# Kernel optimization log

Measured on AMD Instinct MI355X. Metric: run time of the kernel, lower is better.

## Reference

```python
import jax, jax.numpy as jnp
import numpy as np

B, C, H, W = 1, 448, 64, 64
K, M, PAD, STRIDE = 7, 7, 3, 1
CG = C // K          # key/query channels (KeyQueryMap divides by k) = 64
GP_HID = int(0.5 * CG)  # geometry prior hidden channels = 32
K2 = K * K
CENTER = K2 // 2


def conv1x1(x, w, b):
    # x: (B, Cin, H, W), w: (Cout, Cin), b: (Cout,)
    return jnp.einsum('bchw,oc->bohw', x, w) + b[None, :, None, None]


def unfold(x):
    # torch.nn.Unfold(K, dilation=1, padding=PAD, stride=STRIDE)
    # output layout: (B, Cin*K2, L) with dim1 index = c*K2 + (di*K + dj)
    Bc, Cc, Hc, Wc = x.shape
    xp = jnp.pad(x, ((0, 0), (0, 0), (PAD, PAD), (PAD, PAD)))
    Ho = (Hc + 2 * PAD - K) // STRIDE + 1
    Wo = (Wc + 2 * PAD - K) // STRIDE + 1
    patches = [xp[:, :, di:di + Ho * STRIDE:STRIDE, dj:dj + Wo * STRIDE:STRIDE]
               for di in range(K) for dj in range(K)]
    u = jnp.stack(patches, axis=2)  # (B, Cc, K2, Ho, Wo)
    return u.reshape(Bc, Cc * K2, Ho * Wo), Ho, Wo


def geometry_prior(gp_w1, gp_b1, gp_w2, gp_b2):
    ar = jnp.arange(-(K // 2), K // 2 + 1, dtype=jnp.float32)   # -3..3
    x_pos = jnp.broadcast_to(ar[None, :], (K, K))
    y_pos = jnp.broadcast_to(ar[::-1][:, None], (K, K))          # 3..-3 down rows
    pos = jnp.stack([x_pos, y_pos], axis=0)[None]                # (1, 2, K, K)
    h = jax.nn.relu(conv1x1(pos, gp_w1, gp_b1))
    out = conv1x1(h, gp_w2, gp_b2)                               # (1, CG, K, K)
    return out.reshape(1, CG, 1, K2)


def setup_inputs() -> dict:
    key = jax.random.key(0)
    ks = jax.random.split(key, 12)
    def lin(k, cout, cin):
        return jax.random.normal(k, (cout, cin), jnp.float32) / np.sqrt(cin)
    inp = {
        'x': jax.random.normal(ks[0], (B, C, H, W), jnp.float32),
        'Wk': lin(ks[1], CG, C), 'bk': jnp.zeros((CG,), jnp.float32),
        'Wq': lin(ks[2], CG, C), 'bq': jnp.zeros((CG,), jnp.float32),
        'gp_w1': lin(ks[3], GP_HID, 2), 'gp_b1': jax.random.normal(ks[4], (GP_HID,), jnp.float32) * 0.01,
        'gp_w2': lin(ks[5], CG, GP_HID), 'gp_b2': jax.random.normal(ks[6], (CG,), jnp.float32) * 0.01,
        'Wf': lin(ks[7], C, C), 'bf': jnp.zeros((C,), jnp.float32),
    }
    return inp


def reference(x, Wk, bk, Wq, bq, gp_w1, gp_b1, gp_w2, gp_b2, Wf, bf):
    gpk = geometry_prior(gp_w1, gp_b1, gp_w2, gp_b2)        # (1, CG, 1, K2)
    km = conv1x1(x, Wk, bk)                                  # (B, CG, H, W)
    qm = conv1x1(x, Wq, bq)
    ku, Ho, Wo = unfold(km)
    L = Ho * Wo
    ku = ku.reshape(B, CG, L, K2)   # same row-major semantics as torch .view
    qu, _, _ = unfold(qm)
    qu = qu.reshape(B, CG, L, K2)
    ak = ku * qu[:, :, :, CENTER:CENTER + 1]                 # (B, CG, L, K2)
    ck = jax.nn.softmax(ak + gpk, axis=-1)                   # (B, CG, L, K2)
    xu, _, _ = unfold(x)
    xu = xu.reshape(B, M, C // M, L, K2)                     # (B, M, CG, L, K2)
    # ck broadcasts over the M axis (valid since B == 1); sum over window dim
    pre = jnp.einsum('bglp,bmglp->bmgl', ck, xu).reshape(B, C, Ho, Wo)
    return conv1x1(pre, Wf, bf)
```

## Files before the change

### kernel.cpp

```cpp
#include <hip/hip_runtime.h>
#include <hip/hip_bf16.h>

#define CC   448
#define CGC  64
#define MMM  7
#define HWSZ 4096
#define KK2  49
#define GPH  32

typedef __attribute__((ext_vector_type(8))) short   short8;
typedef __attribute__((ext_vector_type(4))) float   f32x4;
typedef __attribute__((ext_vector_type(4))) unsigned short us4;

__device__ __forceinline__ unsigned short f2b(float f) {
    union { __hip_bfloat16 h; unsigned short u; } cv;
    cv.h = __float2bfloat16(f);
    return cv.u;
}

__global__ __launch_bounds__(256) void kq_mfma(
    const float* __restrict__ x,
    const float* __restrict__ Wk, const float* __restrict__ bk,
    const float* __restrict__ Wq, const float* __restrict__ bq,
    float* __restrict__ km, float* __restrict__ qm)
{
    __shared__ unsigned short As[4096];
    __shared__ unsigned short Bs[512];

    const int tid  = threadIdx.x;
    const int nT   = blockIdx.x * 16;
    const int lane = tid & 63;
    const int wid  = tid >> 6;
    const int wm   = wid * 32;
    const int l15  = lane & 15;
    const int l4   = lane >> 4;

    const int ar  = tid >> 3;
    const int ak  = tid & 7;
    const int bkr = tid >> 3;
    const int bn2 = tid & 7;

    f32x4 acc[2];
    acc[0] = (f32x4){0.f, 0.f, 0.f, 0.f};
    acc[1] = (f32x4){0.f, 0.f, 0.f, 0.f};

    float4 a0 = *(const float4*)(Wk + (size_t)ar * CC + ak * 4);
    float4 a1 = *(const float4*)(Wk + (size_t)(ar + 32) * CC + ak * 4);
    float4 a2 = *(const float4*)(Wq + (size_t)ar * CC + ak * 4);
    float4 a3 = *(const float4*)(Wq + (size_t)(ar + 32) * CC + ak * 4);
    float2 b0 = *(const float2*)(x + (size_t)bkr * HWSZ + nT + bn2 * 2);

    for (int kt = 0; kt < 14; ++kt) {
        {
            int kg = ak >> 1, jo = (ak & 1) * 4;
            us4 w;
            w = (us4){ f2b(a0.x), f2b(a0.y), f2b(a0.z), f2b(a0.w) };
            *(us4*)&As[kg * 1024 + (ar +  0) * 8 + jo] = w;
            w = (us4){ f2b(a1.x), f2b(a1.y), f2b(a1.z), f2b(a1.w) };
            *(us4*)&As[kg * 1024 + (ar + 32) * 8 + jo] = w;
            w = (us4){ f2b(a2.x), f2b(a2.y), f2b(a2.z), f2b(a2.w) };
            *(us4*)&As[kg * 1024 + (ar + 64) * 8 + jo] = w;
            w = (us4){ f2b(a3.x), f2b(a3.y), f2b(a3.z), f2b(a3.w) };
            *(us4*)&As[kg * 1024 + (ar + 96) * 8 + jo] = w;
            int base = (bkr >> 3) * 128 + bn2 * 16 + (bkr & 7);
            Bs[base]     = f2b(b0.x);
            Bs[base + 8] = f2b(b0.y);
        }
        __syncthreads();
        if (kt < 13) {
            int ko = (kt + 1) * 32;
            a0 = *(const float4*)(Wk + (size_t)ar * CC + ko + ak * 4);
            a1 = *(const float4*)(Wk + (size_t)(ar + 32) * CC + ko + ak * 4);
            a2 = *(const float4*)(Wq + (size_t)ar * CC + ko + ak * 4);
            a3 = *(const float4*)(Wq + (size_t)(ar + 32) * CC + ko + ak * 4);
            b0 = *(const float2*)(x + (size_t)(ko + bkr) * HWSZ + nT + bn2 * 2);
        }
        short8 fa0 = *(short8*)&As[l4 * 1024 + (wm + l15) * 8];
        short8 fa1 = *(short8*)&As[l4 * 1024 + (wm + 16 + l15) * 8];
        short8 fb0 = *(short8*)&Bs[l4 * 128 + l15 * 8];
        acc[0] = __builtin_amdgcn_mfma_f32_16x16x32_bf16(fa0, fb0, acc[0], 0, 0, 0);
        acc[1] = __builtin_amdgcn_mfma_f32_16x16x32_bf16(fa1, fb0, acc[1], 0, 0, 0);
        __syncthreads();
    }
    const bool isK = (wid < 2);
    float*       Cd   = isK ? km : qm;
    const float* bias = isK ? bk : bq;
    const int rbase = wm & 63;
    #pragma unroll
    for (int wm2 = 0; wm2 < 2; ++wm2)
        #pragma unroll
        for (int r = 0; r < 4; ++r) {
            int row = rbase + wm2 * 16 + l4 * 4 + r;
            int col = nT + l15;
            Cd[(size_t)row * HWSZ + col] = acc[wm2][r] + bias[row];
        }
}

__global__ __launch_bounds__(256) void fconv_mfma(
    const float* __restrict__ pre,
    const float* __restrict__ Wf, const float* __restrict__ bfv,
    float* __restrict__ out)
{
    __shared__ unsigned short As[2048];
    __shared__ unsigned short Bs[1024];

    const int tid  = threadIdx.x;
    const int nT   = blockIdx.x * 32;
    const int oT   = blockIdx.y * 64;
    const int lane = tid & 63;
    const int wid  = tid >> 6;
    const int l15  = lane & 15;
    const int l4   = lane >> 4;

    const int ar  = tid >> 3;
    const int ak  = tid & 7;
    const int bkr = tid >> 3;
    const int bn4 = tid & 7;

    const float* __restrict__ A = Wf + (size_t)oT * CC;

    f32x4 acc[2];
    acc[0] = (f32x4){0.f, 0.f, 0.f, 0.f};
    acc[1] = (f32x4){0.f, 0.f, 0.f, 0.f};

    float4 a0 = *(const float4*)(A + (size_t)ar * CC + ak * 4);
    float4 a1 = *(const float4*)(A + (size_t)(ar + 32) * CC + ak * 4);
    float4 b0 = *(const float4*)(pre + (size_t)bkr * HWSZ + nT + bn4 * 4);

    for (int kt = 0; kt < 14; ++kt) {
        {
            int kg = ak >> 1, jo = (ak & 1) * 4;
            us4 w;
            w = (us4){ f2b(a0.x), f2b(a0.y), f2b(a0.z), f2b(a0.w) };
            *(us4*)&As[kg * 512 + (ar +  0) * 8 + jo] = w;
            w = (us4){ f2b(a1.x), f2b(a1.y), f2b(a1.z), f2b(a1.w) };
            *(us4*)&As[kg * 512 + (ar + 32) * 8 + jo] = w;
            int base = (bkr >> 3) * 256 + bn4 * 32 + (bkr & 7);
            Bs[base]      = f2b(b0.x);
            Bs[base + 8]  = f2b(b0.y);
            Bs[base + 16] = f2b(b0.z);
            Bs[base + 24] = f2b(b0.w);
        }
        __syncthreads();
        if (kt < 13) {
            int ko = (kt + 1) * 32;
            a0 = *(const float4*)(A + (size_t)ar * CC + ko + ak * 4);
            a1 = *(const float4*)(A + (size_t)(ar + 32) * CC + ko + ak * 4);
            b0 = *(const float4*)(pre + (size_t)(ko + bkr) * HWSZ + nT + bn4 * 4);
        }
        short8 fa  = *(short8*)&As[l4 * 512 + (wid * 16 + l15) * 8];
        short8 fb0 = *(short8*)&Bs[l4 * 256 + l15 * 8];
        short8 fb1 = *(short8*)&Bs[l4 * 256 + (16 + l15) * 8];
        acc[0] = __builtin_amdgcn_mfma_f32_16x16x32_bf16(fa, fb0, acc[0], 0, 0, 0);
        acc[1] = __builtin_amdgcn_mfma_f32_16x16x32_bf16(fa, fb1, acc[1], 0, 0, 0);
        __syncthreads();
    }
    #pragma unroll
    for (int wn2 = 0; wn2 < 2; ++wn2)
        #pragma unroll
        for (int r = 0; r < 4; ++r) {
            int row = oT + wid * 16 + l4 * 4 + r;
            int col = nT + wn2 * 16 + l15;
            out[(size_t)row * HWSZ + col] = acc[wn2][r] + bfv[row];
        }
}

#define GLO 196
#define GHI 260
#define XWORDS (GLO + HWSZ + GHI)

__device__ __forceinline__ int win_off_global(int n, bool& ok) {
    int p  = n >> 12;
    int l  = n & 4095;
    int di = (p * 37) >> 8;
    int dj = p - di * 7;
    int i  = (l >> 6) + di - 3;
    int j  = (l & 63) + dj - 3;
    ok = ((unsigned)i < 64u) && ((unsigned)j < 64u);
    return i * 64 + j;
}

__global__ __launch_bounds__(512, 4) void attn_kernel(
    const float* __restrict__ km, const float* __restrict__ qm,
    const float* __restrict__ x,
    const float* __restrict__ gw1, const float* __restrict__ gb1,
    const float* __restrict__ gw2, const float* __restrict__ gb2,
    float* __restrict__ pre)
{
    __shared__ float klin[XWORDS];
    __shared__ float xlin[XWORDS];
    __shared__ float gpk_s[KK2];
    const int tid = threadIdx.x;
    const int g   = blockIdx.y;
    const int lp  = blockIdx.x * 512 + tid;

    if (tid < 114) {
        float4 z = {0.f, 0.f, 0.f, 0.f};
        int w = (tid < 49) ? tid * 4 : (GLO + HWSZ + (tid - 49) * 4);
        *(float4*)&klin[w] = z;
        *(float4*)&xlin[w] = z;
    }
    {
        const float4* km4 = (const float4*)(km + (size_t)g * HWSZ);
        *(float4*)&klin[GLO + tid * 4]         = km4[tid];
        *(float4*)&klin[GLO + (tid + 512) * 4] = km4[tid + 512];
    }
    if (tid < KK2) {
        int di = tid / 7, dj = tid - di * 7;
        float xp = (float)(dj - 3);
        float yp = (float)(3 - di);
        float acc = gb2[g];
        #pragma unroll
        for (int j = 0; j < GPH; ++j) {
            float h = gw1[j * 2 + 0] * xp + gw1[j * 2 + 1] * yp + gb1[j];
            h = fmaxf(h, 0.f);
            acc = fmaf(gw2[g * GPH + j], h, acc);
        }
        gpk_s[tid] = acc;
    }

    float qc;
    { bool ok; int o = win_off_global(lp * KK2 + 24, ok); qc = ok ? qm[(size_t)g * HWSZ + o] : 0.f; }

    const int n0 = lp * KK2;
    const int p0 = n0 >> 12;
    const int l0 = n0 & 4095;
    const int ts = ((p0 + 1) << 12) - n0;
    const int di0 = (p0 * 37) >> 8, dj0 = p0 - di0 * 7;
    const int p1  = p0 + 1;
    const int di1 = (p1 * 37) >> 8, dj1 = p1 - di1 * 7;
    const int djm3_0 = dj0 - 3, djm3_1 = dj1 - 3;
    const int B0 = GLO + l0 + (di0 - 3) * 64 + djm3_0;
    const int B1 = GLO + l0 - 4096 + (di1 - 3) * 64 + djm3_1;

    float4 xr0, xr1;
    {
        const float4* xg4 = (const float4*)(x + (size_t)g * HWSZ);
        xr0 = xg4[tid]; xr1 = xg4[tid + 512];
    }
    __syncthreads();

    float a[KK2];
    float mx = -1e30f;
    #pragma unroll
    for (int t = 0; t < KK2; ++t) {
        bool s1 = (t >= ts);
        int base = s1 ? B1 : B0;
        float kv = klin[base + t];
        int jj = ((l0 + t) & 63) + (s1 ? djm3_1 : djm3_0);
        kv = ((unsigned)jj < 64u) ? kv : 0.f;
        float av = fmaf(kv, qc, gpk_s[t]);
        a[t] = av;
        mx = fmaxf(mx, av);
    }
    float d = 0.f;
    #pragma unroll
    for (int t = 0; t < KK2; ++t) {
        float e = __expf(a[t] - mx);
        d += e;
        bool s1 = (t >= ts);
        int jj = ((l0 + t) & 63) + (s1 ? djm3_1 : djm3_0);
        a[t] = ((unsigned)jj < 64u) ? e : 0.f;
    }
    const float inv = 1.f / d;

    #pragma unroll 1
    for (int m = 0; m < MMM; ++m) {
        __syncthreads();
        *(float4*)&xlin[GLO + tid * 4]         = xr0;
        *(float4*)&xlin[GLO + (tid + 512) * 4] = xr1;
        __syncthreads();
        if (m < MMM - 1) {
            const float4* xg4 = (const float4*)(x + (size_t)((m + 1) * CGC + g) * HWSZ);
            xr0 = xg4[tid]; xr1 = xg4[tid + 512];
        }
        float acc = 0.f;
        #pragma unroll
        for (int t = 0; t < KK2; ++t) {
            int base = (t >= ts) ? B1 : B0;
            acc = fmaf(a[t], xlin[base + t], acc);
        }
        pre[(size_t)(m * CGC + g) * HWSZ + lp] = acc * inv;
    }
}

extern "C" void kernel_launch(void* const* d_in, const int* in_sizes, int n_in,
                              void* d_out, int out_size, void* d_ws, size_t ws_size,
                              hipStream_t stream) {
    const float* x   = (const float*)d_in[0];
    const float* Wk  = (const float*)d_in[1];
    const float* bk  = (const float*)d_in[2];
    const float* Wq  = (const float*)d_in[3];
    const float* bq  = (const float*)d_in[4];
    const float* gw1 = (const float*)d_in[5];
    const float* gb1 = (const float*)d_in[6];
    const float* gw2 = (const float*)d_in[7];
    const float* gb2 = (const float*)d_in[8];
    const float* Wf  = (const float*)d_in[9];
    const float* bfv = (const float*)d_in[10];
    float* out = (float*)d_out;

    float* km  = (float*)d_ws;
    float* qm  = km + CGC * HWSZ;
    float* pre = qm + CGC * HWSZ;

    kq_mfma    <<<dim3(256),    256, 0, stream>>>(x, Wk, bk, Wq, bq, km, qm);
    attn_kernel<<<dim3(8, CGC), 512, 0, stream>>>(km, qm, x, gw1, gb1, gw2, gb2, pre);
    fconv_mfma <<<dim3(128, 7), 256, 0, stream>>>(pre, Wf, bfv, out);
}
```

Baseline: 115.7 us.

## Stage all x channel pages in LDS and fuse softmax with weighted sum

Result: no change. 114.1 us (-1.5%).

```diff
diff --git a/kernel.cpp b/kernel.cpp
--- a/kernel.cpp
+++ b/kernel.cpp
@@ -167,60 +167,60 @@
 
 #define GLO 196
 #define GHI 260
-#define XWORDS (GLO + HWSZ + GHI)
-
-__device__ __forceinline__ int win_off_global(int n, bool& ok) {
-    int p  = n >> 12;
-    int l  = n & 4095;
-    int di = (p * 37) >> 8;
-    int dj = p - di * 7;
-    int i  = (l >> 6) + di - 3;
-    int j  = (l & 63) + dj - 3;
-    ok = ((unsigned)i < 64u) && ((unsigned)j < 64u);
-    return i * 64 + j;
-}
-
-__global__ __launch_bounds__(512, 4) void attn_kernel(
+#define PGW (GLO + HWSZ + GHI)
+#define NPG 8
+
+__global__ __launch_bounds__(1024, 4) void attn_kernel(
     const float* __restrict__ km, const float* __restrict__ qm,
     const float* __restrict__ x,
     const float* __restrict__ gw1, const float* __restrict__ gb1,
     const float* __restrict__ gw2, const float* __restrict__ gb2,
     float* __restrict__ pre)
 {
-    __shared__ float klin[XWORDS];
-    __shared__ float xlin[XWORDS];
+    __shared__ __align__(16) float sm[NPG * PGW];
     __shared__ float gpk_s[KK2];
+
     const int tid = threadIdx.x;
     const int g   = blockIdx.y;
-    const int lp  = blockIdx.x * 512 + tid;
-
-    if (tid < 114) {
-        float4 z = {0.f, 0.f, 0.f, 0.f};
-        int w = (tid < 49) ? tid * 4 : (GLO + HWSZ + (tid - 49) * 4);
-        *(float4*)&klin[w] = z;
-        *(float4*)&xlin[w] = z;
+    const int lp  = blockIdx.x * 1024 + tid;
+
+    if (tid < NPG * 114) {
+        int page = tid / 114;
+        int r    = tid - page * 114;
+        int w    = (r < 49) ? r * 4 : (GLO + HWSZ + (r - 49) * 4);
+        *(float4*)&sm[page * PGW + w] = (float4){0.f, 0.f, 0.f, 0.f};
     }
     {
-        const float4* km4 = (const float4*)(km + (size_t)g * HWSZ);
-        *(float4*)&klin[GLO + tid * 4]         = km4[tid];
-        *(float4*)&klin[GLO + (tid + 512) * 4] = km4[tid + 512];
+        const float4* s0 = (const float4*)(km + (size_t)g * HWSZ);
+        *(float4*)&sm[GLO + tid * 4] = s0[tid];
+        #pragma unroll
+        for (int m = 0; m < MMM; ++m) {
+            const float4* sx = (const float4*)(x + (size_t)(m * CGC + g) * HWSZ);
+            *(float4*)&sm[(m + 1) * PGW + GLO + tid * 4] = sx[tid];
+        }
     }
     if (tid < KK2) {
         int di = tid / 7, dj = tid - di * 7;
         float xp = (float)(dj - 3);
         float yp = (float)(3 - di);
-        float acc = gb2[g];
+        float a2 = gb2[g];
         #pragma unroll
         for (int j = 0; j < GPH; ++j) {
-            float h = gw1[j * 2 + 0] * xp + gw1[j * 2 + 1] * yp + gb1[j];
-            h = fmaxf(h, 0.f);
-            acc = fmaf(gw2[g * GPH + j], h, acc);
-        }
-        gpk_s[tid] = acc;
+            float h = fmaxf(gw1[j * 2 + 0] * xp + gw1[j * 2 + 1] * yp + gb1[j], 0.f);
+            a2 = fmaf(gw2[g * GPH + j], h, a2);
+        }
+        gpk_s[tid] = a2;
     }
 
     float qc;
-    { bool ok; int o = win_off_global(lp * KK2 + 24, ok); qc = ok ? qm[(size_t)g * HWSZ + o] : 0.f; }
+    {
+        int nc = lp * KK2 + 24;
+        int pc = nc >> 12, lc = nc & 4095;
+        int dic = (pc * 37) >> 8, djc = pc - dic * 7;
+        int i = (lc >> 6) + dic - 3, j = (lc & 63) + djc - 3;
+        bool ok = ((unsigned)i < 64u) && ((unsigned)j < 64u);
+        qc = ok ? qm[(size_t)g * HWSZ + i * 64 + j] : 0.f;
+    }
 
     const int n0 = lp * KK2;
     const int p0 = n0 >> 12;
@@ -229,59 +229,82 @@
     const int di0 = (p0 * 37) >> 8, dj0 = p0 - di0 * 7;
     const int p1  = p0 + 1;
     const int di1 = (p1 * 37) >> 8, dj1 = p1 - di1 * 7;
-    const int djm3_0 = dj0 - 3, djm3_1 = dj1 - 3;
-    const int B0 = GLO + l0 + (di0 - 3) * 64 + djm3_0;
-    const int B1 = GLO + l0 - 4096 + (di1 - 3) * 64 + djm3_1;
-
-    float4 xr0, xr1;
+    const int dm0 = dj0 - 3, dm1 = dj1 - 3;
+    const int B0 = GLO + l0 + (di0 - 3) * 64 + dm0;
+    const int B1 = GLO + l0 - HWSZ + (di1 - 3) * 64 + dm1;
+    const int c0 = l0 + (dm0 > 0 ? dm0 : 0), w0 = (dm0 < 0) ? -dm0 : dm0;
+    const int c1 = l0 + (dm1 > 0 ? dm1 : 0), w1 = (dm1 < 0) ? -dm1 : dm1;
+
+    __syncthreads();
+
+    float d = 0.f;
+    float acc[MMM];
+    #pragma unroll
+    for (int m = 0; m < MMM; ++m) acc[m] = 0.f;
+
+    #pragma unroll
+    for (int tp = 0; tp < 24; ++tp) {
+        const int t0 = 2 * tp, t1 = t0 + 1;
+        const bool s1 = (t1 >= ts);
+        const int bb = s1 ? B1 : B0;
+        const int cc = s1 ? c1 : c0;
+        const int ww = s1 ? w1 : w0;
+        float kv0 = sm[bb + t0];
+        float kv1 = sm[bb + t1];
+        const bool bad0 = (((cc + t0) & 63) < ww);
+        const bool bad1 = (((cc + t1) & 63) < ww);
+        kv0 = bad0 ? 0.f : kv0;
+        kv1 = bad1 ? 0.f : kv1;
+        const float e0 = __expf(fmaf(kv0, qc, gpk_s[t0]));
+        const float e1 = __expf(fmaf(kv1, qc, gpk_s[t1]));
+        d += e0 + e1;
+        const float em0 = bad0 ? 0.f : e0;
+        const float em1 = bad1 ? 0.f : e1;
+        #pragma unroll
+        for (int m = 0; m < MMM; ++m) {
+            const int ob = bb + (m + 1) * PGW;
+            acc[m] = fmaf(em1, sm[ob + t1], fmaf(em0, sm[ob + t0], acc[m]));
+        }
+    }
     {
-        const float4* xg4 = (const float4*)(x + (size_t)g * HWSZ);
-        xr0 = xg4[tid]; xr1 = xg4[tid + 512];
-    }
-    __syncthreads();
-
-    float a[KK2];
-    float mx = -1e30f;
-    #pragma unroll
-    for (int t = 0; t < KK2; ++t) {
-        bool s1 = (t >= ts);
-        int base = s1 ? B1 : B0;
-        float kv = klin[base + t];
-        int jj = ((l0 + t) & 63) + (s1 ? djm3_1 : djm3_0);
-        kv = ((unsigned)jj < 64u) ? kv : 0.f;
-        float av = fmaf(kv, qc, gpk_s[t]);
-        a[t] = av;
-        mx = fmaxf(mx, av);
-    }
-    float d = 0.f;
-    #pragma unroll
-    for (int t = 0; t < KK2; ++t) {
-        float e = __expf(a[t] - mx);
+        const bool s1 = (48 >= ts);
+        const int bb = s1 ? B1 : B0;
+        const int cc = s1 ? c1 : c0;
+        const int ww = s1 ? w1 : w0;
+        float kv = sm[bb + 48];
+        const bool bad = (((cc + 48) & 63) < ww);
+        kv = bad ? 0.f : kv;
+        const float e = __expf(fmaf(kv, qc, gpk_s[48]));
         d += e;
-        bool s1 = (t >= ts);
-        int jj = ((l0 + t) & 63) + (s1 ? djm3_1 : djm3_0);
-        a[t] = ((unsigned)jj < 64u) ? e : 0.f;
-    }
+        const float em = bad ? 0.f : e;
+        #pragma unroll
+        for (int m = 0; m < MMM; ++m)
+            acc[m] = fmaf(em, sm[bb + (m + 1) * PGW + 48], acc[m]);
+    }
+    if (ts < 49 && (ts & 1)) {
+        const int tw = ts - 1;
+        const float gw = gpk_s[tw];
+        float kw = sm[B1 + tw];
+        const bool bw = (((c1 + tw) & 63) < w1);
+        kw = bw ? 0.f : kw;
+        const float ew  = __expf(fmaf(kw, qc, gw));
+        const float emw = bw ? 0.f : ew;
+        float kr = sm[B0 + tw];
+        const bool br = (((c0 + tw) & 63) < w0);
+        kr = br ? 0.f : kr;
+        const float er  = __expf(fmaf(kr, qc, gw));
+        const float emr = br ? 0.f : er;
+        d += er - ew;
+        #pragma unroll
+        for (int m = 0; m < MMM; ++m)
+            acc[m] += emr * sm[B0 + (m + 1) * PGW + tw]
+                    - emw * sm[B1 + (m + 1) * PGW + tw];
+    }
+
     const float inv = 1.f / d;
-
-    #pragma unroll 1
-    for (int m = 0; m < MMM; ++m) {
-        __syncthreads();
-        *(float4*)&xlin[GLO + tid * 4]         = xr0;
-        *(float4*)&xlin[GLO + (tid + 512) * 4] = xr1;
-        __syncthreads();
-        if (m < MMM - 1) {
-            const float4* xg4 = (const float4*)(x + (size_t)((m + 1) * CGC + g) * HWSZ);
-            xr0 = xg4[tid]; xr1 = xg4[tid + 512];
-        }
-        float acc = 0.f;
-        #pragma unroll
-        for (int t = 0; t < KK2; ++t) {
-            int base = (t >= ts) ? B1 : B0;
-            acc = fmaf(a[t], xlin[base + t], acc);
-        }
-        pre[(size_t)(m * CGC + g) * HWSZ + lp] = acc * inv;
-    }
+    #pragma unroll
+    for (int m = 0; m < MMM; ++m)
+        pre[(size_t)(m * CGC + g) * HWSZ + lp] = acc[m] * inv;
 }
 
 extern "C" void kernel_launch(void* const* d_in, const int* in_sizes, int n_in,
@@ -305,6 +328,6 @@
     float* pre = qm + CGC * HWSZ;
 
     kq_mfma    <<<dim3(256),    256, 0, stream>>>(x, Wk, bk, Wq, bq, km, qm);
-    attn_kernel<<<dim3(8, CGC), 512, 0, stream>>>(km, qm, x, gw1, gb1, gw2, gb2, pre);
+    attn_kernel<<<dim3(4, CGC), 1024, 0, stream>>>(km, qm, x, gw1, gb1, gw2, gb2, pre);
     fconv_mfma <<<dim3(128, 7), 256, 0, stream>>>(pre, Wf, bfv, out);
 }
```
